# Kernel optimization log

Hardware: AMD Instinct MI355X
Metric: run time of the kernel (lower is better)

## Reference

```python
import jax, jax.numpy as jnp
import numpy as np

N_NODES = 2048
N_EDGES = 32768
DIM = 256
HEADS = 4

PARAM_SHAPES = {
    'Wq': (DIM, DIM), 'bq': (DIM,), 'Wk': (DIM, DIM), 'bk': (DIM,),
    'Wv': (DIM, DIM), 'bv': (DIM,), 'Wo': (DIM, DIM), 'bo': (DIM,),
    'gd_W1': (4, 3), 'gd_b1': (3,), 'gd_W2': (3, HEADS), 'gd_b2': (HEADS,),
    'tw_W1': (2 * DIM, DIM), 'tw_b1': (DIM,), 'tw_W2': (DIM, DIM), 'tw_b2': (DIM,),
    'ne_W1': (4 * DIM, 2 * DIM), 'ne_b1': (2 * DIM,), 'ne_W2': (2 * DIM, DIM), 'ne_b2': (DIM,),
    'att_W1': (2 * DIM // HEADS, 2 * DIM // HEADS), 'att_b1': (2 * DIM // HEADS,),
    'att_W2': (DIM // HEADS, 2 * DIM // HEADS), 'att_b2': (DIM // HEADS,),
    'pe_W': (DIM, DIM), 'pe_b': (DIM,), 'pq_W': (DIM, DIM), 'pq_b': (DIM,),
    'pv_W': (DIM, DIM), 'pv_b': (DIM,),
    'pr_W1': (2 * DIM, 2 * DIM), 'pr_b1': (2 * DIM,), 'pr_W2': (2 * DIM, DIM), 'pr_b2': (DIM,),
}


def _lin(x, W, b):
    return x @ W + b


def _mlp2(x, W1, b1, W2, b2):  # Linear-ReLU-Linear (build_mlp, on_last=False)
    return _lin(jnp.maximum(_lin(x, W1, b1), 0.0), W2, b2)


def setup_inputs() -> dict:
    key = jax.random.key(0)
    ks = iter(jax.random.split(key, 64))
    rng = np.random.default_rng(0)
    half = N_EDGES // 2
    s = rng.integers(0, N_NODES, half)
    d = rng.integers(0, N_NODES, half)
    # reciprocal edge pairs so the reverse-edge lookup path is exercised
    edge_index = jnp.asarray(np.stack([np.concatenate([s, d]), np.concatenate([d, s])]), dtype=jnp.int32)
    inp = {
        'node_f': jax.random.normal(next(ks), (N_NODES, DIM), jnp.float32),
        'edge_f': jax.random.normal(next(ks), (N_EDGES, DIM), jnp.float32),
        'coords': jax.random.normal(next(ks), (N_NODES, 3), jnp.float32),
        'edge_index': edge_index,
        'num_heads': HEADS,
    }
    for name, shp in PARAM_SHAPES.items():
        inp[name] = jax.random.normal(next(ks), shp, jnp.float32) * 0.02
    return inp


def _forward(node_f, edge_f, coords, edge_index, num_heads,
             Wq, bq, Wk, bk, Wv, bv, Wo, bo,
             gd_W1, gd_b1, gd_W2, gd_b2,
             tw_W1, tw_b1, tw_W2, tw_b2,
             ne_W1, ne_b1, ne_W2, ne_b2,
             att_W1, att_b1, att_W2, att_b2,
             pe_W, pe_b, pq_W, pq_b, pv_W, pv_b,
             pr_W1, pr_b1, pr_W2, pr_b2):
    N, Dn = node_f.shape
    E, De = edge_f.shape
    H = num_heads
    dh = Wq.shape[1] // H
    src, dst = edge_index[0], edge_index[1]

    # --- NodeUpdate: distance-aware MHSA over all node pairs (batch=1) ---
    q = _lin(node_f, Wq, bq).reshape(N, H, dh)
    k = _lin(node_f, Wk, bk).reshape(N, H, dh)
    v = _lin(node_f, Wv, bv).reshape(N, H, dh)
    diff = coords[:, None, :] - coords[None, :, :]  # [N,N,3]
    sq = jnp.sum(diff * diff, axis=-1, keepdims=True)
    dist = jnp.where(sq > 0, jnp.sqrt(jnp.where(sq > 0, sq, 1.0)), 0.0)
    dmask = _mlp2(jnp.concatenate([diff, dist], -1), gd_W1, gd_b1, gd_W2, gd_b2)  # [N,N,H]
    scores = jnp.einsum('nhd,mhd->hnm', q, k) / float(dh) ** 0.5 + dmask.transpose(2, 0, 1)
    attn = jax.nn.softmax(scores, axis=-1)
    mhsa = _lin(jnp.einsum('hnm,mhd->nhd', attn, v).reshape(N, H * dh), Wo, bo)

    # --- TwinningEdgeAttention: per-node mean of outgoing / incoming edge feats ---
    ones = jnp.ones((E,), edge_f.dtype)
    cnt_s = jnp.maximum(jax.ops.segment_sum(ones, src, num_segments=N), 1.0)
    cnt_d = jnp.maximum(jax.ops.segment_sum(ones, dst, num_segments=N), 1.0)
    sub_mean = jax.ops.segment_sum(edge_f, src, num_segments=N) / cnt_s[:, None]
    obj_mean = jax.ops.segment_sum(edge_f, dst, num_segments=N) / cnt_d[:, None]
    edge_att = jax.nn.sigmoid(_mlp2(jnp.concatenate([sub_mean, obj_mean], -1), tw_W1, tw_b1, tw_W2, tw_b2))
    node_out = jnp.maximum(mhsa, 0.0) * edge_att  # [N, Dn]

    # --- GraphEdgeAttenNetwork ---
    x_i = node_f[src]
    x_j = node_f[dst]
    # reverse-edge matching (vectorized replacement of the python double loop)
    table = jnp.zeros((N * N,), jnp.int32).at[src * N + dst].set(jnp.arange(E, dtype=jnp.int32) + 1)
    rev = table[dst * N + src]
    rev_feat = jnp.where((rev > 0)[:, None], edge_f[jnp.maximum(rev - 1, 0)], 0.0)
    edge_out = _mlp2(jnp.concatenate([x_i, edge_f, rev_feat, x_j], -1), ne_W1, ne_b1, ne_W2, ne_b2)

    value = _lin(x_j, pv_W, pv_b)  # [E, Da]
    query = _lin(x_i, pq_W, pq_b).reshape(E, Dn // H, H)
    edgep = _lin(edge_f, pe_W, pe_b).reshape(E, De // H, H)
    qe = jnp.concatenate([query, edgep], axis=1)  # [E, d_n+d_e, H]
    # conv1d(kernel=1) MLP over channel axis, ReLU between layers
    h = jnp.maximum(jnp.einsum('ech,oc->eoh', qe, att_W1) + att_b1[None, :, None], 0.0)
    prob = jax.nn.softmax(jnp.einsum('ech,oc->eoh', h, att_W2) + att_b2[None, :, None], axis=1)  # [E, d_o, H]
    msg = prob.reshape(E, -1) * value
    agg = jax.ops.segment_max(msg, src, num_segments=N)
    agg = jnp.where(jnp.isfinite(agg), agg, 0.0)  # empty segments -> 0 (torch scatter_max fill)
    xx = _mlp2(jnp.concatenate([node_f, agg], -1), pr_W1, pr_b1, pr_W2, pr_b2)
    return node_out, edge_out, xx


def reference(node_f, edge_f, coords, edge_index, num_heads,
              Wq, bq, Wk, bk, Wv, bv, Wo, bo,
              gd_W1, gd_b1, gd_W2, gd_b2,
              tw_W1, tw_b1, tw_W2, tw_b2,
              ne_W1, ne_b1, ne_W2, ne_b2,
              att_W1, att_b1, att_W2, att_b2,
              pe_W, pe_b, pq_W, pq_b, pv_W, pv_b,
              pr_W1, pr_b1, pr_W2, pr_b2):
    return _forward(node_f, edge_f, coords, edge_index, num_heads,
                    Wq, bq, Wk, bk, Wv, bv, Wo, bo,
                    gd_W1, gd_b1, gd_W2, gd_b2,
                    tw_W1, tw_b1, tw_W2, tw_b2,
                    ne_W1, ne_b1, ne_W2, ne_b2,
                    att_W1, att_b1, att_W2, att_b2,
                    pe_W, pe_b, pq_W, pq_b, pv_W, pv_b,
                    pr_W1, pr_b1, pr_W2, pr_b2)
```

## Files before the change

### kernel.cpp

```cpp
#include <hip/hip_runtime.h>

#define NN 2048
#define NE 32768
#define DIM 256
#define NH 4

typedef unsigned short u16;
typedef __attribute__((ext_vector_type(4))) unsigned short u16x4;
typedef __attribute__((ext_vector_type(8))) short bf16x8;
typedef __attribute__((ext_vector_type(4))) float f32x4;

typedef __attribute__((address_space(1))) const unsigned int g_as1;
typedef __attribute__((address_space(3))) unsigned int l_as3;

__device__ __forceinline__ void gload16(const u16* g, u16* l) {
  __builtin_amdgcn_global_load_lds((g_as1*)g, (l_as3*)l, 16, 0, 0);
}

__device__ __forceinline__ u16 f2bf(float f) {
  unsigned u = __float_as_uint(f);
  unsigned r = u + 0x7FFFu + ((u >> 16) & 1u);
  return (u16)(r >> 16);
}
__device__ __forceinline__ float bf2f(u16 b) {
  return __uint_as_float(((unsigned)b) << 16);
}

struct GB { const u16* A; const int* idx; long ld; long aoffz; };

template<int BNF, int EPI>
__global__ __launch_bounds__(256) void gemm_bf(
    GB ga, const u16* __restrict__ Bt, long bld, long boffz,
    const float* __restrict__ bias, void* __restrict__ Cp, long ldc, long coffz,
    int K, float scale)
{
  __shared__ u16 As[128 * 64];
  __shared__ u16 Bs[32 * BNF * 64];

  const int tid = threadIdx.x;
  const int wid = tid >> 6, lane = tid & 63;
  const int bz = blockIdx.z;
  const int m0 = blockIdx.y * 128;
  const int n0 = blockIdx.x * (32 * BNF);
  const int wr = wid >> 1, wc = wid & 1;
  const int l15 = lane & 15, l4 = lane >> 4;

  const u16* asrc[4];
  #pragma unroll
  for (int c = 0; c < 4; ++c) {
    int rl = c*32 + wid*8 + (lane >> 3);
    int row = ga.idx ? ga.idx[m0 + rl] : (m0 + rl);
    int c16s = (lane & 7) ^ (rl & 7);
    asrc[c] = ga.A + ga.aoffz * bz + (long)row * ga.ld + c16s * 8;
  }
  const u16* bsrc[BNF];
  #pragma unroll
  for (int c = 0; c < BNF; ++c) {
    int rl = c*32 + wid*8 + (lane >> 3);
    int c16s = (lane & 7) ^ (rl & 7);
    bsrc[c] = Bt + boffz * bz + (long)(n0 + rl) * bld + c16s * 8;
  }

  f32x4 acc[4][BNF] = {};

  for (int k0 = 0; k0 < K; k0 += 64) {
    #pragma unroll
    for (int c = 0; c < 4; ++c)
      gload16(asrc[c] + k0, &As[(c*32 + wid*8) * 64]);
    #pragma unroll
    for (int c = 0; c < BNF; ++c)
      gload16(bsrc[c] + k0, &Bs[(c*32 + wid*8) * 64]);
    __syncthreads();

    #pragma unroll
    for (int kk = 0; kk < 2; ++kk) {
      bf16x8 af[4], bfr[BNF];
      #pragma unroll
      for (int i = 0; i < 4; ++i) {
        int r = wr*64 + i*16 + l15;
        af[i] = *(const bf16x8*)&As[r*64 + (((kk*4 + l4) ^ (r & 7)) * 8)];
      }
      #pragma unroll
      for (int j = 0; j < BNF; ++j) {
        int r = wc*(16*BNF) + j*16 + l15;
        bfr[j] = *(const bf16x8*)&Bs[r*64 + (((kk*4 + l4) ^ (r & 7)) * 8)];
      }
      #pragma unroll
      for (int i = 0; i < 4; ++i)
        #pragma unroll
        for (int j = 0; j < BNF; ++j)
          acc[i][j] = __builtin_amdgcn_mfma_f32_16x16x32_bf16(af[i], bfr[j], acc[i][j], 0, 0, 0);
    }
    __syncthreads();
  }

  #pragma unroll
  for (int j = 0; j < BNF; ++j) {
    const int col = n0 + wc*(16*BNF) + j*16 + l15;
    const float bb = bias ? bias[col] : 0.f;
    #pragma unroll
    for (int i = 0; i < 4; ++i) {
      #pragma unroll
      for (int r = 0; r < 4; ++r) {
        const int m = m0 + wr*64 + i*16 + l4*4 + r;
        float v = acc[i][j][r] * scale + bb;
        if constexpr (EPI == 1) v = fmaxf(v, 0.f);
        if constexpr (EPI == 2) v = 1.f / (1.f + expf(-v));
        if constexpr (EPI == 0 || EPI == 2)
          ((float*)Cp)[coffz*bz + (long)m*ldc + col] = v;
        else if constexpr (EPI == 4)
          ((u16*)Cp)[((long)(col & 3) * NE + m) * ldc + (col >> 2) + coffz] = f2bf(v);
        else if constexpr (EPI == 8) {
          if (col < 256)
            ((float*)Cp)[(long)m*256 + (col & 3)*64 + (col >> 2)] = v;
          else {
            u16* qb = (u16*)((float*)Cp + (long)NN*256);
            int c2 = col - 256;
            qb[((long)(c2 & 3)*NN + m)*64 + (c2 >> 2)] = f2bf(v);
          }
        }
        else
          ((u16*)Cp)[coffz*bz + (long)m*ldc + col] = f2bf(v);
      }
    }
  }
}

__global__ __launch_bounds__(256) void flash_k(
    const u16* __restrict__ qkv,
    const u16* __restrict__ vT,
    const float4* __restrict__ pk,
    const float* __restrict__ gW1, const float* __restrict__ gb1,
    const float* __restrict__ gW2, const float* __restrict__ gb2,
    float* __restrict__ Op,
    float2* __restrict__ ml)
{
  __shared__ u16 Qls[64*64];
  __shared__ u16 Kls[128*64];
  __shared__ u16 Vls[2][64*64];
  __shared__ u16 Pls[4][16*128];

  const int tid = threadIdx.x, wid = tid >> 6, lane = tid & 63;
  const int h  = blockIdx.x & 3;
  const int m0 = (blockIdx.x >> 2) * 64;
  const int part = blockIdx.y;
  const int l15 = lane & 15, l4 = lane >> 4;
  const int rl8 = wid*8 + (lane >> 3);
  const int c8  = lane & 7;

  #pragma unroll
  for (int c = 0; c < 2; ++c) {
    int r = c*32 + rl8;
    gload16(qkv + (long)(m0 + r)*768 + h*64 + ((c8 ^ (r & 7))*8), &Qls[(c*32 + wid*8)*64]);
  }
  __syncthreads();
  bf16x8 qf[2];
  {
    int r = wid*16 + l15;
    qf[0] = *(const bf16x8*)&Qls[r*64 + (((0*4 + l4) ^ (r & 7))*8)];
    qf[1] = *(const bf16x8*)&Qls[r*64 + (((1*4 + l4) ^ (r & 7))*8)];
  }

  const float b10 = gb1[0], b11 = gb1[1], b12 = gb1[2];
  const float w30 = gW1[9], w31 = gW1[10], w32 = gW1[11];
  const float w20 = gW2[0*4+h], w21 = gW2[1*4+h], w22 = gW2[2*4+h];
  const float b2h = gb2[h];
  float4 rp0[4], rp1[4];
  #pragma unroll
  for (int r = 0; r < 4; ++r) {
    int qrow = m0 + wid*16 + l4*4 + r;
    rp0[r] = pk[qrow*2]; rp1[r] = pk[qrow*2 + 1];
  }

  float mrun[4] = {-1e30f, -1e30f, -1e30f, -1e30f};
  float lrun[4] = {};
  f32x4 pa[4] = {};

  for (int t = 0; t < 2; ++t) {
    const int n0 = part*256 + t*128;
    #pragma unroll
    for (int c = 0; c < 4; ++c) {
      int r = c*32 + rl8;
      gload16(qkv + (long)(n0 + r)*768 + 256 + h*64 + ((c8 ^ (r & 7))*8),
              &Kls[(c*32 + wid*8)*64]);
    }
    #pragma unroll
    for (int hh = 0; hh < 2; ++hh)
      #pragma unroll
      for (int c = 0; c < 2; ++c) {
        int r = c*32 + rl8;
        gload16(vT + (long)(h*64 + r)*NN + n0 + hh*64 + ((c8 ^ (r & 7))*8),
                &Vls[hh][(c*32 + wid*8)*64]);
      }
    __syncthreads();

    f32x4 sa[8] = {};
    #pragma unroll
    for (int kk = 0; kk < 2; ++kk) {
      #pragma unroll
      for (int j = 0; j < 8; ++j) {
        int r = j*16 + l15;
        bf16x8 bf = *(const bf16x8*)&Kls[r*64 + (((kk*4 + l4) ^ (r & 7))*8)];
        sa[j] = __builtin_amdgcn_mfma_f32_16x16x32_bf16(qf[kk], bf, sa[j], 0, 0, 0);
      }
    }

    float rowmx[4] = {-1e30f, -1e30f, -1e30f, -1e30f};
    #pragma unroll
    for (int j = 0; j < 8; ++j) {
      int n = n0 + j*16 + l15;
      float4 cp0 = pk[n*2], cp1 = pk[n*2 + 1];
      #pragma unroll
      for (int r = 0; r < 4; ++r) {
        float dot = rp0[r].x*cp0.x + rp0[r].y*cp0.y + rp0[r].z*cp0.z;
        float sq = rp0[r].w + cp0.w - 2.f*dot;
        float dist = sq > 0.f ? sq * __frsqrt_rn(sq) : 0.f;
        float h0 = fmaxf(b10 + rp1[r].x - cp1.x + dist*w30, 0.f);
        float h1 = fmaxf(b11 + rp1[r].y - cp1.y + dist*w31, 0.f);
        float h2 = fmaxf(b12 + rp1[r].z - cp1.z + dist*w32, 0.f);
        float s = sa[j][r]*0.125f + b2h + h0*w20 + h1*w21 + h2*w22;
        sa[j][r] = s;
        rowmx[r] = fmaxf(rowmx[r], s);
      }
    }
    #pragma unroll
    for (int w = 1; w < 16; w <<= 1)
      #pragma unroll
      for (int r = 0; r < 4; ++r)
        rowmx[r] = fmaxf(rowmx[r], __shfl_xor(rowmx[r], w));

    float fac[4], rs[4] = {};
    #pragma unroll
    for (int r = 0; r < 4; ++r) {
      float mnew = fmaxf(mrun[r], rowmx[r]);
      fac[r] = __expf(mrun[r] - mnew);
      mrun[r] = mnew;
    }
    #pragma unroll
    for (int j = 0; j < 8; ++j)
      #pragma unroll
      for (int r = 0; r < 4; ++r) {
        float p = __expf(sa[j][r] - mrun[r]);
        sa[j][r] = p;
        rs[r] += p;
      }
    #pragma unroll
    for (int w = 1; w < 16; w <<= 1)
      #pragma unroll
      for (int r = 0; r < 4; ++r)
        rs[r] += __shfl_xor(rs[r], w);
    #pragma unroll
    for (int r = 0; r < 4; ++r) lrun[r] = lrun[r]*fac[r] + rs[r];
    #pragma unroll
    for (int j2 = 0; j2 < 4; ++j2)
      #pragma unroll
      for (int r = 0; r < 4; ++r)
        pa[j2][r] *= fac[r];

    #pragma unroll
    for (int j = 0; j < 8; ++j)
      #pragma unroll
      for (int r = 0; r < 4; ++r) {
        int qr = l4*4 + r, n = j*16 + l15;
        Pls[wid][qr*128 + (((n >> 3) ^ (qr & 7))*8) + (n & 7)] = f2bf(sa[j][r]);
      }
    #pragma unroll
    for (int ks = 0; ks < 4; ++ks) {
      bf16x8 paf = *(const bf16x8*)&Pls[wid][l15*128 + (((ks*4 + l4) ^ (l15 & 7))*8)];
      #pragma unroll
      for (int j2 = 0; j2 < 4; ++j2) {
        int r = j2*16 + l15;
        bf16x8 vf = *(const bf16x8*)&Vls[ks >> 1][r*64 + ((((ks & 1)*4 + l4) ^ (r & 7))*8)];
        pa[j2] = __builtin_amdgcn_mfma_f32_16x16x32_bf16(paf, vf, pa[j2], 0, 0, 0);
      }
    }
    __syncthreads();
  }

  #pragma unroll
  for (int j2 = 0; j2 < 4; ++j2)
    #pragma unroll
    for (int r = 0; r < 4; ++r) {
      int m = m0 + wid*16 + l4*4 + r;
      Op[((long)part*NN + m)*256 + h*64 + j2*16 + l15] = pa[j2][r];
    }
  if (l15 == 0) {
    #pragma unroll
    for (int r = 0; r < 4; ++r) {
      int m = m0 + wid*16 + l4*4 + r;
      ml[((long)part*NN + m)*4 + h] = make_float2(mrun[r], lrun[r]);
    }
  }
}

__global__ __launch_bounds__(256) void comb_k(const float* __restrict__ Op,
    const float2* __restrict__ ml, u16* __restrict__ attn) {
  int n = blockIdx.x, t = threadIdx.x, h = t >> 6;
  float m[8], l[8];
  #pragma unroll
  for (int p = 0; p < 8; ++p) { float2 v = ml[((long)p*NN + n)*4 + h]; m[p] = v.x; l[p] = v.y; }
  float M = m[0];
  #pragma unroll
  for (int p = 1; p < 8; ++p) M = fmaxf(M, m[p]);
  float L = 0.f, o = 0.f;
  #pragma unroll
  for (int p = 0; p < 8; ++p) {
    float w = __expf(m[p] - M);
    L += w * l[p];
    o += w * Op[((long)p*NN + n)*256 + t];
  }
  attn[(long)n*256 + t] = f2bf(o / L);
}

__global__ __launch_bounds__(64) void attedge_k(
    const u16* __restrict__ qN, const u16* __restrict__ ep,
    const float* __restrict__ valNp, const int* __restrict__ ei,
    const u16* __restrict__ W1, const float* __restrict__ b1,
    const u16* __restrict__ W2, const float* __restrict__ b2,
    u16* __restrict__ msgP)
{
  __shared__ u16 As[32*128];
  const int lane = threadIdx.x;
  const int h = blockIdx.y;
  const int e0 = blockIdx.x * 32;
  const int l15 = lane & 15, l4 = lane >> 4;

  #pragma unroll
  for (int p = 0; p < 8; ++p) {
    int R0 = p*4;
    int r  = R0 + (lane >> 4);
    int cd = lane & 15;
    int cs = ((cd & 7) ^ (r & 7)) | (cd & 8);
    const u16* src = (cs < 8)
        ? qN + ((long)h*NN + ei[e0 + r])*64 + cs*8
        : ep + ((long)h*NE + e0 + r)*64 + (cs & 7)*8;
    gload16(src, &As[R0*128]);
  }
  __syncthreads();

  f32x4 acc1[2][8] = {};
  #pragma unroll
  for (int kk = 0; kk < 4; ++kk) {
    bf16x8 af[2], bfr[8];
    #pragma unroll
    for (int i = 0; i < 2; ++i) {
      int rA = i*16 + l15;
      int cg = kk*4 + l4;
      int cd = ((cg & 7) ^ (rA & 7)) | (cg & 8);
      af[i] = *(const bf16x8*)&As[rA*128 + cd*8];
    }
    #pragma unroll
    for (int j = 0; j < 8; ++j)
      bfr[j] = *(const bf16x8*)&W1[(long)(j*16 + l15)*128 + kk*32 + l4*8];
    #pragma unroll
    for (int i = 0; i < 2; ++i)
      #pragma unroll
      for (int j = 0; j < 8; ++j)
        acc1[i][j] = __builtin_amdgcn_mfma_f32_16x16x32_bf16(af[i], bfr[j], acc1[i][j], 0, 0, 0);
  }
  __syncthreads();
  #pragma unroll
  for (int i = 0; i < 2; ++i)
    #pragma unroll
    for (int j = 0; j < 8; ++j) {
      int n = j*16 + l15;
      float bb = b1[n];
      #pragma unroll
      for (int r = 0; r < 4; ++r) {
        int m = i*16 + l4*4 + r;
        int cg = n >> 3;
        int cd = ((cg & 7) ^ (m & 7)) | (cg & 8);
        As[m*128 + cd*8 + (n & 7)] = f2bf(fmaxf(acc1[i][j][r] + bb, 0.f));
      }
    }
  __syncthreads();

  f32x4 acc2[2][4] = {};
  #pragma unroll
  for (int kk = 0; kk < 4; ++kk) {
    bf16x8 af[2], bfr[4];
    #pragma unroll
    for (int i = 0; i < 2; ++i) {
      int rA = i*16 + l15;
      int cg = kk*4 + l4;
      int cd = ((cg & 7) ^ (rA & 7)) | (cg & 8);
      af[i] = *(const bf16x8*)&As[rA*128 + cd*8];
    }
    #pragma unroll
    for (int j = 0; j < 4; ++j)
      bfr[j] = *(const bf16x8*)&W2[(long)(j*16 + l15)*128 + kk*32 + l4*8];
    #pragma unroll
    for (int i = 0; i < 2; ++i)
      #pragma unroll
      for (int j = 0; j < 4; ++j)
        acc2[i][j] = __builtin_amdgcn_mfma_f32_16x16x32_bf16(af[i], bfr[j], acc2[i][j], 0, 0, 0);
  }

  #pragma unroll
  for (int i = 0; i < 2; ++i) {
    float mx[4] = {-1e30f,-1e30f,-1e30f,-1e30f};
    #pragma unroll
    for (int j = 0; j < 4; ++j) {
      float bb = b2[j*16 + l15];
      #pragma unroll
      for (int r = 0; r < 4; ++r) {
        acc2[i][j][r] += bb;
        mx[r] = fmaxf(mx[r], acc2[i][j][r]);
      }
    }
    #pragma unroll
    for (int w = 1; w < 16; w <<= 1)
      #pragma unroll
      for (int r = 0; r < 4; ++r) mx[r] = fmaxf(mx[r], __shfl_xor(mx[r], w));
    float sum[4] = {};
    #pragma unroll
    for (int j = 0; j < 4; ++j)
      #pragma unroll
      for (int r = 0; r < 4; ++r) {
        float p = __expf(acc2[i][j][r] - mx[r]);
        acc2[i][j][r] = p; sum[r] += p;
      }
    #pragma unroll
    for (int w = 1; w < 16; w <<= 1)
      #pragma unroll
      for (int r = 0; r < 4; ++r) sum[r] += __shfl_xor(sum[r], w);
    #pragma unroll
    for (int r = 0; r < 4; ++r) {
      int m = i*16 + l4*4 + r;
      int e = e0 + m;
      int dst = ei[NE + e];
      float inv = 1.f / sum[r];
      #pragma unroll
      for (int j = 0; j < 4; ++j) {
        int o = j*16 + l15;
        float v = valNp[(long)dst*256 + h*64 + o];
        msgP[(long)e*256 + h*64 + o] = f2bf(acc2[i][j][r] * inv * v);
      }
    }
  }
}

__global__ __launch_bounds__(256) void gemm_ne(
    const u16* __restrict__ nbf, const u16* __restrict__ ebf, const u16* __restrict__ zbuf,
    const int* __restrict__ ei, const int* __restrict__ rev,
    const u16* __restrict__ Bt, const float* __restrict__ bias, u16* __restrict__ C)
{
  __shared__ u16 As[2][128 * 64];
  __shared__ u16 Bs[2][128 * 64];
  const int tid = threadIdx.x, wid = tid >> 6, lane = tid & 63;
  const int lin = blockIdx.y * 4 + blockIdx.x;
  const int xcd = lin & 7, seq = lin >> 3;
  const int m0 = (xcd*32 + (seq >> 2)) * 128;
  const int n0 = (seq & 3) * 128;
  const int wr = wid >> 1, wc = wid & 1, l15 = lane & 15, l4 = lane >> 4;

  const u16* asrc[4][4];
  #pragma unroll
  for (int c = 0; c < 4; ++c) {
    int rl = c*32 + wid*8 + (lane >> 3);
    int m = m0 + rl;
    int c16s = ((lane & 7) ^ (rl & 7)) * 8;
    int si = ei[m], di = ei[NE + m], rv = rev[m];
    asrc[0][c] = nbf + (long)si * 256 + c16s;
    asrc[1][c] = ebf + (long)m * 256 + c16s;
    asrc[2][c] = (rv >= 0 ? ebf + (long)rv * 256 : zbuf) + c16s;
    asrc[3][c] = nbf + (long)di * 256 + c16s;
  }
  const u16* bsrc[4];
  #pragma unroll
  for (int c = 0; c < 4; ++c) {
    int rl = c*32 + wid*8 + (lane >> 3);
    int c16s = (lane & 7) ^ (rl & 7);
    bsrc[c] = Bt + (long)(n0 + rl) * 1024 + c16s * 8;
  }

  f32x4 acc[4][4] = {};

#define NE_STAGE(BUF, IT) do {                                                  \
    const int seg_ = (IT) >> 2, kt_ = (IT) & 3;                                 \
    _Pragma("unroll")                                                           \
    for (int c = 0; c < 4; ++c)                                                 \
      gload16(asrc[seg_][c] + kt_*64, &As[BUF][(c*32 + wid*8) * 64]);           \
    _Pragma("unroll")                                                           \
    for (int c = 0; c < 4; ++c)                                                 \
      gload16(bsrc[c] + seg_*256 + kt_*64, &Bs[BUF][(c*32 + wid*8) * 64]);      \
  } while (0)

  NE_STAGE(0, 0);
  #pragma unroll
  for (int it = 0; it < 16; ++it) {
    const int b = it & 1;
    if (it < 15) {
      NE_STAGE(b ^ 1, it + 1);
      asm volatile("s_waitcnt vmcnt(8)" ::: "memory");
    } else {
      asm volatile("s_waitcnt vmcnt(0)" ::: "memory");
    }
    __builtin_amdgcn_s_barrier();
    asm volatile("" ::: "memory");
    #pragma unroll
    for (int kk = 0; kk < 2; ++kk) {
      bf16x8 af[4], bfr[4];
      #pragma unroll
      for (int i = 0; i < 4; ++i) {
        int r = wr*64 + i*16 + l15;
        af[i] = *(const bf16x8*)&As[b][r*64 + (((kk*4 + l4) ^ (r & 7)) * 8)];
      }
      #pragma unroll
      for (int j = 0; j < 4; ++j) {
        int r = wc*64 + j*16 + l15;
        bfr[j] = *(const bf16x8*)&Bs[b][r*64 + (((kk*4 + l4) ^ (r & 7)) * 8)];
      }
      #pragma unroll
      for (int i = 0; i < 4; ++i)
        #pragma unroll
        for (int j = 0; j < 4; ++j)
          acc[i][j] = __builtin_amdgcn_mfma_f32_16x16x32_bf16(af[i], bfr[j], acc[i][j], 0, 0, 0);
    }
    asm volatile("" ::: "memory");
    __builtin_amdgcn_s_barrier();
  }
#undef NE_STAGE

  #pragma unroll
  for (int j = 0; j < 4; ++j) {
    const int col = n0 + wc*64 + j*16 + l15;
    const float bb = bias[col];
    #pragma unroll
    for (int i = 0; i < 4; ++i) {
      #pragma unroll
      for (int r = 0; r < 4; ++r) {
        const int m = m0 + wr*64 + i*16 + l4*4 + r;
        C[(long)m*512 + col] = f2bf(fmaxf(acc[i][j][r] + bb, 0.f));
      }
    }
  }
}

struct PrepEnt { const float* src; void* dst; int K; int N; int ntiles; int op; };
struct PrepDesc { PrepEnt e[24]; int n; };

__global__ __launch_bounds__(256) void wprep_k(PrepDesc d) {
  __shared__ float t[32][33];
  int b = blockIdx.x;
  int ei = 0;
  while (ei < d.n && b >= d.e[ei].ntiles) { b -= d.e[ei].ntiles; ++ei; }
  if (ei >= d.n) return;
  PrepEnt E = d.e[ei];
  int tid = threadIdx.x;
  if (E.op == 0) {
    int kt = E.K >> 5;
    int bk = (b % kt) * 32, bn = (b / kt) * 32;
    int tx = tid & 31, ty = tid >> 5;
    #pragma unroll
    for (int i = ty; i < 32; i += 8) t[i][tx] = E.src[(long)(bk + i) * E.N + bn + tx];
    __syncthreads();
    u16* dst = (u16*)E.dst;
    #pragma unroll
    for (int i = ty; i < 32; i += 8) dst[(long)(bn + i) * E.K + bk + tx] = f2bf(t[tx][i]);
  } else if (E.op == 1) {
    long i = (long)b * 256 + tid;
    long n4 = ((long)E.K * E.N) >> 2;
    if (i < n4) {
      float4 v = ((const float4*)E.src)[i];
      u16x4 o = { f2bf(v.x), f2bf(v.y), f2bf(v.z), f2bf(v.w) };
      ((u16x4*)E.dst)[i] = o;
    }
  } else if (E.op == 3) {
    long i = (long)b * 256 + tid;
    long n4 = ((long)E.K * E.N) >> 2;
    if (i < n4) {
      float4 v = ((const float4*)E.src)[i];
      long row = i >> 6;
      long col = (i & 63) * 4;
      u16x4 o = { f2bf(v.x), f2bf(v.y), f2bf(v.z), f2bf(v.w) };
      *(u16x4*)((u16*)E.dst + row*512 + col) = o;
    }
  } else {
    int i = b * 256 + tid;
    if (i < E.N) ((float*)E.dst)[i] = E.src[i];
  }
}

__global__ void geo_k(const float* __restrict__ C3, const float* __restrict__ gW1,
                      float* __restrict__ geo) {
  int n = blockIdx.x * 256 + threadIdx.x;
  if (n >= NN) return;
  float cx = C3[3*n], cy = C3[3*n+1], cz = C3[3*n+2];
  float s = cx*cx + cy*cy + cz*cz;
  float a0 = cx*gW1[0] + cy*gW1[3] + cz*gW1[6];
  float a1 = cx*gW1[1] + cy*gW1[4] + cz*gW1[7];
  float a2 = cx*gW1[2] + cy*gW1[5] + cz*gW1[8];
  float4* g = (float4*)(geo + (long)n*8);
  g[0] = make_float4(cx, cy, cz, s);
  g[1] = make_float4(a0, a1, a2, 0.f);
}

__global__ __launch_bounds__(256) void transb_k(const u16* __restrict__ src,
                                                u16* __restrict__ dst) {
  __shared__ u16 t[32][34];
  int bm = blockIdx.x * 32, bc = blockIdx.y * 32;
  int tx = threadIdx.x & 31, ty = threadIdx.x >> 5;
  #pragma unroll
  for (int i = ty; i < 32; i += 8) t[i][tx] = src[(long)(bm+i)*768 + 512 + bc + tx];
  __syncthreads();
  #pragma unroll
  for (int i = ty; i < 32; i += 8) dst[(long)(bc+i)*NN + bm + tx] = t[tx][i];
}

__global__ __launch_bounds__(256) void seg_sum_k(const float* __restrict__ ef,
    const int* __restrict__ ei, float* sub, float* obj, float* cs, float* cd) {
  int e = blockIdx.x * 4 + (threadIdx.x >> 6);
  int lane = threadIdx.x & 63;
  int s = ei[e], d = ei[NE + e];
  const float* row = ef + (long)e * DIM;
  #pragma unroll
  for (int c = 0; c < 4; ++c) {
    float v = row[lane + c*64];
    atomicAdd(&sub[(long)s*DIM + lane + c*64], v);
    atomicAdd(&obj[(long)d*DIM + lane + c*64], v);
  }
  if (lane == 0) { atomicAdd(&cs[s], 1.f); atomicAdd(&cd[d], 1.f); }
}

__global__ void pack_tw_k(const float* __restrict__ sub, const float* __restrict__ obj,
    const float* __restrict__ cs, const float* __restrict__ cd, u16* __restrict__ twA) {
  int n = blockIdx.x, t = threadIdx.x;
  int seg = t >> 6, c = (t & 63) * 4;
  float sc = seg ? 1.f / fmaxf(cd[n], 1.f) : 1.f / fmaxf(cs[n], 1.f);
  float4 v = *(const float4*)((seg ? obj : sub) + (long)n * DIM + c);
  u16x4 o = { f2bf(v.x*sc), f2bf(v.y*sc), f2bf(v.z*sc), f2bf(v.w*sc) };
  *(u16x4*)&twA[(long)n*512 + seg*256 + c] = o;
}

__global__ void node_out_k(const float* mh, const float* ea, float* out) {
  long i = (long)blockIdx.x * 256 + threadIdx.x;
  out[i] = fmaxf(mh[i], 0.f) * ea[i];
}

__global__ void scat_k(const int* ei, int* tbl) {
  int e = blockIdx.x * 256 + threadIdx.x;
  atomicMax(&tbl[(long)ei[e] * NN + ei[NE + e]], e + 1);
}

__global__ void rev_k(const int* ei, const int* tbl, int* rev) {
  int e = blockIdx.x * 256 + threadIdx.x;
  rev[e] = tbl[(long)ei[NE + e] * NN + ei[e]] - 1;
}

__global__ __launch_bounds__(256) void scan_k(const float* __restrict__ cs,
    int* __restrict__ start, int* __restrict__ cursor) {
  __shared__ int part[256];
  int t = threadIdx.x;
  int loc[8]; int s = 0;
  #pragma unroll
  for (int i = 0; i < 8; ++i) { int v = (int)cs[t*8 + i]; loc[i] = s; s += v; }
  part[t] = s;
  __syncthreads();
  if (t == 0) { int a = 0; for (int i = 0; i < 256; ++i) { int v = part[i]; part[i] = a; a += v; } }
  __syncthreads();
  int base = part[t];
  #pragma unroll
  for (int i = 0; i < 8; ++i) { start[t*8+i] = base + loc[i]; cursor[t*8+i] = base + loc[i]; }
  if (t == 255) start[2048] = base + s;
}

__global__ void scatter_k(const int* __restrict__ ei, int* __restrict__ cursor,
                          int* __restrict__ eids) {
  int e = blockIdx.x * 256 + threadIdx.x;
  int pos = atomicAdd(&cursor[ei[e]], 1);
  eids[pos] = e;
}

__global__ __launch_bounds__(256) void agg_k(const int* __restrict__ start,
    const int* __restrict__ eids, const u16* __restrict__ msgP, u16* __restrict__ prA) {
  int n = blockIdx.x, t = threadIdx.x;
  int b = start[n], e_ = start[n+1];
  float mx = -1e30f;
  for (int i = b; i < e_; ++i) {
    int e = eids[i];
    mx = fmaxf(mx, bf2f(msgP[(long)e*256 + t]));
  }
  int c = (t & 63) * 4 + (t >> 6);
  prA[(long)n*512 + 256 + c] = (e_ > b) ? f2bf(mx) : f2bf(0.f);
}

static GB gb(const u16* A, const int* idx, long ld, long aoffz) {
  GB g; g.A = A; g.idx = idx; g.ld = ld; g.aoffz = aoffz; return g;
}

extern "C" void kernel_launch(void* const* d_in, const int* in_sizes, int n_in,
                              void* d_out, int out_size, void* d_ws, size_t ws_size,
                              hipStream_t stream) {
  (void)in_sizes; (void)n_in; (void)out_size; (void)ws_size;

  const float* node_f = (const float*)d_in[0];
  const float* edge_f = (const float*)d_in[1];
  const float* coords = (const float*)d_in[2];
  const int*   ei     = (const int*)d_in[3];
  const float* Wq = (const float*)d_in[5];  const float* bq = (const float*)d_in[6];
  const float* Wk = (const float*)d_in[7];  const float* bk = (const float*)d_in[8];
  const float* Wv = (const float*)d_in[9];  const float* bv = (const float*)d_in[10];
  const float* Wo = (const float*)d_in[11]; const float* bo = (const float*)d_in[12];
  const float* gd_W1 = (const float*)d_in[13]; const float* gd_b1 = (const float*)d_in[14];
  const float* gd_W2 = (const float*)d_in[15]; const float* gd_b2 = (const float*)d_in[16];
  const float* tw_W1 = (const float*)d_in[17]; const float* tw_b1 = (const float*)d_in[18];
  const float* tw_W2 = (const float*)d_in[19]; const float* tw_b2 = (const float*)d_in[20];
  const float* ne_W1 = (const float*)d_in[21]; const float* ne_b1 = (const float*)d_in[22];
  const float* ne_W2 = (const float*)d_in[23]; const float* ne_b2 = (const float*)d_in[24];
  const float* att_W1 = (const float*)d_in[25]; const float* att_b1 = (const float*)d_in[26];
  const float* att_W2 = (const float*)d_in[27]; const float* att_b2 = (const float*)d_in[28];
  const float* pe_W = (const float*)d_in[29]; const float* pe_b = (const float*)d_in[30];
  const float* pq_W = (const float*)d_in[31]; const float* pq_b = (const float*)d_in[32];
  const float* pv_W = (const float*)d_in[33]; const float* pv_b = (const float*)d_in[34];
  const float* pr_W1 = (const float*)d_in[35]; const float* pr_b1 = (const float*)d_in[36];
  const float* pr_W2 = (const float*)d_in[37]; const float* pr_b2 = (const float*)d_in[38];

  char* WB = (char*)d_ws;
  float* out = (float*)d_out;
  float* out_node = out;
  float* out_edge = out + (long)NN*DIM;
  float* out_xx   = out + (long)NN*DIM + (long)NE*DIM;

  const long sz_R1 = 4L*NN*NN*4;
  const long sz_R2 = 4L*NN*NN*2;
  const long sz_R3 = 4L*NE*128*2;
  const long R1 = 0, R2 = R1 + sz_R1, R3 = R2 + sz_R2;

  float*  Opart = (float*)(WB + R1);
  float2* mlbuf = (float2*)(WB + R1 + 8L*NN*256*4);
  u16*    msgP  = (u16*)(WB + R1);
  u16*   nehid  = (u16*)(WB + R2);
  int*   tbl    = (int*)(WB + R3);
  u16*   ep     = (u16*)(WB + R3);
  u16*   edge_bf= (u16*)(WB + R3 + (long)NN*NN*4);

  long cur = R3 + sz_R3;
  auto alloc = [&](long bytes) { long o = cur; cur += (bytes + 255) & ~255L; return o; };

  long o_sub = alloc(2L*NN*DIM*4);
  float* sub = (float*)(WB + o_sub);
  float* obj = sub + (long)NN*DIM;
  u16* qkv_bf  = (u16*)sub;
  u16* vT      = (u16*)obj;
  u16* attn_bf = vT + (long)NN*DIM;

  long o_cs  = alloc(2L*NN*4);
  float* cs = (float*)(WB + o_cs); float* cd = cs + NN;
  long o_mh  = alloc((long)NN*DIM*4);  float* mhsa = (float*)(WB + o_mh);
  long o_ea  = alloc((long)NN*DIM*4);  float* eatt = (float*)(WB + o_ea);
  long o_rv  = alloc((long)NE*4);      int* rev = (int*)(WB + o_rv);
  long o_st  = alloc((NN+1)*4);        int* startp = (int*)(WB + o_st);
  long o_cu  = alloc(NN*4);            int* cursor = (int*)(WB + o_cu);
  long o_eid = alloc((long)NE*4);      int* eids = (int*)(WB + o_eid);
  long o_zb  = alloc(1024);            u16* zbuf = (u16*)(WB + o_zb);
  long o_geo = alloc((long)NN*8*4);    float* geo = (float*)(WB + o_geo);
  long o_nbf = alloc((long)NN*DIM*2);  u16* node_bf = (u16*)(WB + o_nbf);
  long o_twA = alloc((long)NN*512*2);  u16* twA = (u16*)(WB + o_twA);
  long o_twh = alloc((long)NN*DIM*2);  u16* twh = (u16*)(WB + o_twh);
  long o_prA = alloc((long)NN*512*2);  u16* prA = (u16*)(WB + o_prA);
  long o_prh = alloc((long)NN*512*2);  u16* prh = (u16*)(WB + o_prh);
  long o_vN  = alloc((long)NN*256*4 + 4L*NN*64*2);
  float* valN = (float*)(WB + o_vN);
  u16*   qN   = (u16*)(valN + (long)NN*256);

  u16* qkv_t = (u16*)(WB + alloc(3L*DIM*DIM*2));
  u16* Wo_t  = (u16*)(WB + alloc(DIM*DIM*2));
  u16* tw1_t = (u16*)(WB + alloc(DIM*512*2));
  u16* tw2_t = (u16*)(WB + alloc(DIM*DIM*2));
  u16* ne1_t = (u16*)(WB + alloc(512L*1024*2));
  u16* ne2_t = (u16*)(WB + alloc(DIM*512*2));
  u16* pe_t  = (u16*)(WB + alloc(DIM*DIM*2));
  u16* pvq_t = (u16*)(WB + alloc(2L*DIM*DIM*2));
  u16* pr1_t = (u16*)(WB + alloc(512L*512*2));
  u16* pr2_t = (u16*)(WB + alloc(DIM*512*2));
  u16* a1_bf = (u16*)(WB + alloc(128*128*2));
  u16* a2_bf = (u16*)(WB + alloc(64*128*2));
  float* qkvb = (float*)(WB + alloc(768*4));
  float* pvqb = (float*)(WB + alloc(512*4));

  hipMemsetAsync(sub, 0, 2L*NN*DIM*4, stream);
  hipMemsetAsync(cs, 0, 2L*NN*4, stream);
  hipMemsetAsync(tbl, 0, (long)NN*NN*4, stream);
  hipMemsetAsync(zbuf, 0, 1024, stream);

  PrepDesc pd{}; int ne_ = 0; int tot = 0;
  auto addT = [&](const float* s, u16* d, int K, int N) {
    pd.e[ne_] = { s, d, K, N, (K/32)*(N/32), 0 }; tot += pd.e[ne_].ntiles; ++ne_;
  };
  auto addC = [&](const float* s, u16* d, long elems) {
    int nt = (int)((elems/4 + 255) / 256);
    pd.e[ne_] = { s, d, 1, (int)elems, nt, 1 }; tot += nt; ++ne_;
  };
  auto addB = [&](const float* s, float* d, int n) {
    pd.e[ne_] = { s, d, 1, n, (n + 255)/256, 2 }; tot += pd.e[ne_].ntiles; ++ne_;
  };
  addT(Wq, qkv_t,               DIM, DIM);
  addT(Wk, qkv_t + DIM*DIM,     DIM, DIM);
  addT(Wv, qkv_t + 2*DIM*DIM,   DIM, DIM);
  addT(Wo, Wo_t, DIM, DIM);
  addT(tw_W1, tw1_t, 512, DIM);
  addT(tw_W2, tw2_t, DIM, DIM);
  addT(ne_W1, ne1_t, 1024, 512);
  addT(ne_W2, ne2_t, 512, DIM);
  addT(pe_W, pe_t, DIM, DIM);
  addT(pv_W, pvq_t,             DIM, DIM);
  addT(pq_W, pvq_t + DIM*DIM,   DIM, DIM);
  addT(pr_W1, pr1_t, 512, 512);
  addT(pr_W2, pr2_t, 512, DIM);
  addC(att_W1, a1_bf, 128*128);
  addC(att_W2, a2_bf, 64*128);
  addC(node_f, node_bf, (long)NN*DIM);
  addC(edge_f, edge_bf, (long)NE*DIM);
  addB(bq, qkvb, 256); addB(bk, qkvb + 256, 256); addB(bv, qkvb + 512, 256);
  addB(pv_b, pvqb, 256); addB(pq_b, pvqb + 256, 256);
  pd.e[ne_] = { node_f, prA, NN, 256, (int)(((long)NN*256/4 + 255)/256), 3 };
  tot += pd.e[ne_].ntiles; ++ne_;
  pd.n = ne_;
  wprep_k<<<tot, 256, 0, stream>>>(pd);
  geo_k<<<NN/256, 256, 0, stream>>>(coords, gd_W1, geo);

  seg_sum_k<<<NE/4, 256, 0, stream>>>(edge_f, ei, sub, obj, cs, cd);
  scan_k<<<1, 256, 0, stream>>>(cs, startp, cursor);
  scatter_k<<<NE/256, 256, 0, stream>>>(ei, cursor, eids);
  pack_tw_k<<<NN, 128, 0, stream>>>(sub, obj, cs, cd, twA);
  gemm_bf<4,1><<<dim3(2,16,1), 256, 0, stream>>>(gb(twA, nullptr, 512, 0), tw1_t, 512, 0,
      tw_b1, twh, DIM, 0, 512, 1.f);
  gemm_bf<4,2><<<dim3(2,16,1), 256, 0, stream>>>(gb(twh, nullptr, DIM, 0), tw2_t, DIM, 0,
      tw_b2, eatt, DIM, 0, DIM, 1.f);

  gemm_bf<4,5><<<dim3(6,16,1), 256, 0, stream>>>(gb(node_bf, nullptr, DIM, 0), qkv_t, DIM, 0,
      qkvb, qkv_bf, 768, 0, DIM, 1.f);
  transb_k<<<dim3(64,8), 256, 0, stream>>>(qkv_bf, vT);
  flash_k<<<dim3(128,8), 256, 0, stream>>>(qkv_bf, vT, (const float4*)geo,
      gd_W1, gd_b1, gd_W2, gd_b2, Opart, mlbuf);
  comb_k<<<NN, 256, 0, stream>>>(Opart, mlbuf, attn_bf);
  gemm_bf<4,0><<<dim3(2,16,1), 256, 0, stream>>>(gb(attn_bf, nullptr, DIM, 0), Wo_t, DIM, 0,
      bo, mhsa, DIM, 0, DIM, 1.f);
  node_out_k<<<NN, 256, 0, stream>>>(mhsa, eatt, out_node);

  scat_k<<<NE/256, 256, 0, stream>>>(ei, tbl);
  rev_k<<<NE/256, 256, 0, stream>>>(ei, tbl, rev);
  gemm_ne<<<dim3(4,256,1), 256, 0, stream>>>(node_bf, edge_bf, zbuf, ei, rev,
      ne1_t, ne_b1, nehid);
  gemm_bf<4,0><<<dim3(2,256,1), 256, 0, stream>>>(gb(nehid, nullptr, 512, 0), ne2_t, 512, 0,
      ne_b2, out_edge, DIM, 0, 512, 1.f);

  gemm_bf<4,8><<<dim3(4,16,1), 256, 0, stream>>>(gb(node_bf, nullptr, DIM, 0), pvq_t, DIM, 0,
      pvqb, valN, 256, 0, DIM, 1.f);
  gemm_bf<4,4><<<dim3(2,256,1), 256, 0, stream>>>(gb(edge_bf, nullptr, DIM, 0), pe_t, DIM, 0,
      pe_b, ep, 64, 0, DIM, 1.f);
  attedge_k<<<dim3(NE/32, NH), 64, 0, stream>>>(qN, ep, valN, ei,
      a1_bf, att_b1, a2_bf, att_b2, msgP);
  agg_k<<<NN, 256, 0, stream>>>(startp, eids, msgP, prA);

  gemm_bf<4,1><<<dim3(4,16,1), 256, 0, stream>>>(gb(prA, nullptr, 512, 0), pr1_t, 512, 0,
      pr_b1, prh, 512, 0, 512, 1.f);
  gemm_bf<4,0><<<dim3(2,16,1), 256, 0, stream>>>(gb(prh, nullptr, 512, 0), pr2_t, 512, 0,
      pr_b2, out_xx, DIM, 0, 512, 1.f);
}
```

Before: 433.9 us.

## Replace atomic float scatter-add segment means with CSR gather over bf16 edges

Replaces the per-edge float atomicAdd scatter into src/dst sums with integer counting, two CSR scans (source and destination), and a per-node gather kernel that sums bf16 edge features and divides by count. This removes 16M float atomics and the 4MB memset plus pack pass, and reuses the existing edge_bf copy. It trades that for reading bf16-rounded inputs, a serial per-node loop, and extra scatter and scan work for destination lists. The qkv/vT buffers are re-laid out inside the freed space.

```diff
diff --git a/kernel.cpp b/kernel.cpp
--- a/kernel.cpp
+++ b/kernel.cpp
@@ -608,53 +608,23 @@
   for (int i = ty; i < 32; i += 8) dst[(long)(bc+i)*NN + bm + tx] = t[tx][i];
 }
 
-__global__ __launch_bounds__(256) void seg_sum_k(const float* __restrict__ ef,
-    const int* __restrict__ ei, float* sub, float* obj, float* cs, float* cd) {
-  int e = blockIdx.x * 4 + (threadIdx.x >> 6);
-  int lane = threadIdx.x & 63;
-  int s = ei[e], d = ei[NE + e];
-  const float* row = ef + (long)e * DIM;
-  #pragma unroll
-  for (int c = 0; c < 4; ++c) {
-    float v = row[lane + c*64];
-    atomicAdd(&sub[(long)s*DIM + lane + c*64], v);
-    atomicAdd(&obj[(long)d*DIM + lane + c*64], v);
-  }
-  if (lane == 0) { atomicAdd(&cs[s], 1.f); atomicAdd(&cd[d], 1.f); }
-}
-
-__global__ void pack_tw_k(const float* __restrict__ sub, const float* __restrict__ obj,
-    const float* __restrict__ cs, const float* __restrict__ cd, u16* __restrict__ twA) {
-  int n = blockIdx.x, t = threadIdx.x;
-  int seg = t >> 6, c = (t & 63) * 4;
-  float sc = seg ? 1.f / fmaxf(cd[n], 1.f) : 1.f / fmaxf(cs[n], 1.f);
-  float4 v = *(const float4*)((seg ? obj : sub) + (long)n * DIM + c);
-  u16x4 o = { f2bf(v.x*sc), f2bf(v.y*sc), f2bf(v.z*sc), f2bf(v.w*sc) };
-  *(u16x4*)&twA[(long)n*512 + seg*256 + c] = o;
-}
-
-__global__ void node_out_k(const float* mh, const float* ea, float* out) {
-  long i = (long)blockIdx.x * 256 + threadIdx.x;
-  out[i] = fmaxf(mh[i], 0.f) * ea[i];
-}
-
-__global__ void scat_k(const int* ei, int* tbl) {
+__global__ void count_k(const int* __restrict__ ei, int* __restrict__ cs,
+                        int* __restrict__ cd) {
   int e = blockIdx.x * 256 + threadIdx.x;
-  atomicMax(&tbl[(long)ei[e] * NN + ei[NE + e]], e + 1);
-}
-
-__global__ void rev_k(const int* ei, const int* tbl, int* rev) {
-  int e = blockIdx.x * 256 + threadIdx.x;
-  rev[e] = tbl[(long)ei[NE + e] * NN + ei[e]] - 1;
-}
-
-__global__ __launch_bounds__(256) void scan_k(const float* __restrict__ cs,
-    int* __restrict__ start, int* __restrict__ cursor) {
+  atomicAdd(&cs[ei[e]], 1);
+  atomicAdd(&cd[ei[NE + e]], 1);
+}
+
+__global__ __launch_bounds__(256) void scan2_k(const int* __restrict__ cnt_all,
+    int* __restrict__ start_all, int* __restrict__ cursor_all) {
+  const int* cnt = cnt_all + blockIdx.x * NN;
+  int* start  = start_all + blockIdx.x * (NN + 1);
+  int* cursor = cursor_all + blockIdx.x * NN;
   __shared__ int part[256];
   int t = threadIdx.x;
   int loc[8]; int s = 0;
   #pragma unroll
-  for (int i = 0; i < 8; ++i) { int v = (int)cs[t*8 + i]; loc[i] = s; s += v; }
+  for (int i = 0; i < 8; ++i) { int v = cnt[t*8 + i]; loc[i] = s; s += v; }
   part[t] = s;
   __syncthreads();
   if (t == 0) { int a = 0; for (int i = 0; i < 256; ++i) { int v = part[i]; part[i] = a; a += v; } }
@@ -662,14 +632,49 @@
   int base = part[t];
   #pragma unroll
   for (int i = 0; i < 8; ++i) { start[t*8+i] = base + loc[i]; cursor[t*8+i] = base + loc[i]; }
-  if (t == 255) start[2048] = base + s;
-}
-
-__global__ void scatter_k(const int* __restrict__ ei, int* __restrict__ cursor,
-                          int* __restrict__ eids) {
+  if (t == 255) start[NN] = base + s;
+}
+
+__global__ void scatter2_k(const int* __restrict__ ei, int* __restrict__ cur_s,
+    int* __restrict__ cur_d, int* __restrict__ eids_s, int* __restrict__ eids_d) {
   int e = blockIdx.x * 256 + threadIdx.x;
-  int pos = atomicAdd(&cursor[ei[e]], 1);
-  eids[pos] = e;
+  int p = atomicAdd(&cur_s[ei[e]], 1);
+  eids_s[p] = e;
+  int q = atomicAdd(&cur_d[ei[NE + e]], 1);
+  eids_d[q] = e;
+}
+
+__global__ __launch_bounds__(256) void twmean_k(const u16* __restrict__ ebf,
+    const int* __restrict__ start_s, const int* __restrict__ eids_s,
+    const int* __restrict__ start_d, const int* __restrict__ eids_d,
+    u16* __restrict__ twA)
+{
+  int n = blockIdx.x, t = threadIdx.x;
+  int b0 = start_s[n], e0 = start_s[n+1];
+  float s = 0.f;
+  for (int i = b0; i < e0; ++i)
+    s += bf2f(ebf[(long)eids_s[i]*256 + t]);
+  twA[(long)n*512 + t] = f2bf(s / fmaxf((float)(e0 - b0), 1.f));
+  int b1 = start_d[n], e1 = start_d[n+1];
+  float s2 = 0.f;
+  for (int i = b1; i < e1; ++i)
+    s2 += bf2f(ebf[(long)eids_d[i]*256 + t]);
+  twA[(long)n*512 + 256 + t] = f2bf(s2 / fmaxf((float)(e1 - b1), 1.f));
+}
+
+__global__ void node_out_k(const float* mh, const float* ea, float* out) {
+  long i = (long)blockIdx.x * 256 + threadIdx.x;
+  out[i] = fmaxf(mh[i], 0.f) * ea[i];
+}
+
+__global__ void scat_k(const int* ei, int* tbl) {
+  int e = blockIdx.x * 256 + threadIdx.x;
+  atomicMax(&tbl[(long)ei[e] * NN + ei[NE + e]], e + 1);
+}
+
+__global__ void rev_k(const int* ei, const int* tbl, int* rev) {
+  int e = blockIdx.x * 256 + threadIdx.x;
+  rev[e] = tbl[(long)ei[NE + e] * NN + ei[e]] - 1;
 }
 
 __global__ __launch_bounds__(256) void agg_k(const int* __restrict__ start,
@@ -739,20 +744,21 @@
   auto alloc = [&](long bytes) { long o = cur; cur += (bytes + 255) & ~255L; return o; };
 
   long o_sub = alloc(2L*NN*DIM*4);
-  float* sub = (float*)(WB + o_sub);
-  float* obj = sub + (long)NN*DIM;
-  u16* qkv_bf  = (u16*)sub;
-  u16* vT      = (u16*)obj;
+  u16* qkv_bf  = (u16*)(WB + o_sub);
+  u16* vT      = qkv_bf + (long)NN*768;
   u16* attn_bf = vT + (long)NN*DIM;
 
   long o_cs  = alloc(2L*NN*4);
-  float* cs = (float*)(WB + o_cs); float* cd = cs + NN;
+  int* cs_i = (int*)(WB + o_cs); int* cd_i = cs_i + NN;
   long o_mh  = alloc((long)NN*DIM*4);  float* mhsa = (float*)(WB + o_mh);
   long o_ea  = alloc((long)NN*DIM*4);  float* eatt = (float*)(WB + o_ea);
   long o_rv  = alloc((long)NE*4);      int* rev = (int*)(WB + o_rv);
-  long o_st  = alloc((NN+1)*4);        int* startp = (int*)(WB + o_st);
-  long o_cu  = alloc(NN*4);            int* cursor = (int*)(WB + o_cu);
-  long o_eid = alloc((long)NE*4);      int* eids = (int*)(WB + o_eid);
+  long o_st  = alloc(2L*(NN+1)*4);     int* start_s = (int*)(WB + o_st);
+  int* start_d = start_s + (NN + 1);
+  long o_cu  = alloc(2L*NN*4);         int* cursor_s = (int*)(WB + o_cu);
+  int* cursor_d = cursor_s + NN;
+  long o_eid = alloc(2L*NE*4);         int* eids_s = (int*)(WB + o_eid);
+  int* eids_d = eids_s + NE;
   long o_zb  = alloc(1024);            u16* zbuf = (u16*)(WB + o_zb);
   long o_geo = alloc((long)NN*8*4);    float* geo = (float*)(WB + o_geo);
   long o_nbf = alloc((long)NN*DIM*2);  u16* node_bf = (u16*)(WB + o_nbf);
@@ -779,8 +785,7 @@
   float* qkvb = (float*)(WB + alloc(768*4));
   float* pvqb = (float*)(WB + alloc(512*4));
 
-  hipMemsetAsync(sub, 0, 2L*NN*DIM*4, stream);
-  hipMemsetAsync(cs, 0, 2L*NN*4, stream);
+  hipMemsetAsync(cs_i, 0, 2L*NN*4, stream);
   hipMemsetAsync(tbl, 0, (long)NN*NN*4, stream);
   hipMemsetAsync(zbuf, 0, 1024, stream);
 
@@ -820,10 +825,10 @@
   wprep_k<<<tot, 256, 0, stream>>>(pd);
   geo_k<<<NN/256, 256, 0, stream>>>(coords, gd_W1, geo);
 
-  seg_sum_k<<<NE/4, 256, 0, stream>>>(edge_f, ei, sub, obj, cs, cd);
-  scan_k<<<1, 256, 0, stream>>>(cs, startp, cursor);
-  scatter_k<<<NE/256, 256, 0, stream>>>(ei, cursor, eids);
-  pack_tw_k<<<NN, 128, 0, stream>>>(sub, obj, cs, cd, twA);
+  count_k<<<NE/256, 256, 0, stream>>>(ei, cs_i, cd_i);
+  scan2_k<<<2, 256, 0, stream>>>(cs_i, start_s, cursor_s);
+  scatter2_k<<<NE/256, 256, 0, stream>>>(ei, cursor_s, cursor_d, eids_s, eids_d);
+  twmean_k<<<NN, 256, 0, stream>>>(edge_bf, start_s, eids_s, start_d, eids_d, twA);
   gemm_bf<4,1><<<dim3(2,16,1), 256, 0, stream>>>(gb(twA, nullptr, 512, 0), tw1_t, 512, 0,
       tw_b1, twh, DIM, 0, 512, 1.f);
   gemm_bf<4,2><<<dim3(2,16,1), 256, 0, stream>>>(gb(twh, nullptr, DIM, 0), tw2_t, DIM, 0,
@@ -852,7 +857,7 @@
       pe_b, ep, 64, 0, DIM, 1.f);
   attedge_k<<<dim3(NE/32, NH), 64, 0, stream>>>(qN, ep, valN, ei,
       a1_bf, att_b1, a2_bf, att_b2, msgP);
-  agg_k<<<NN, 256, 0, stream>>>(startp, eids, msgP, prA);
+  agg_k<<<NN, 256, 0, stream>>>(start_s, eids_s, msgP, prA);
 
   gemm_bf<4,1><<<dim3(4,16,1), 256, 0, stream>>>(gb(prA, nullptr, 512, 0), pr1_t, 512, 0,
       pr_b1, prh, 512, 0, 512, 1.f);
```

Result: faster. 398.4 us (-8.2%).
